# Optimization experiments

Measured on AMD Instinct MI355X. Metric: run time of the kernel, lower is better.

Reference implementation:

```python
import jax, jax.numpy as jnp
import numpy as np

B, T, E, H = 4, 2048, 4096, 128

def setup_inputs() -> dict:
    key = jax.random.key(0)
    ks = jax.random.split(key, 5)
    x = jax.random.normal(ks[0], (B, T, E), dtype=jnp.float32)
    pos_emb = jax.random.normal(ks[1], (B, T, E), dtype=jnp.float32)
    # torch nn.Linear(E, H, bias=False) weights have shape [H, E]
    scale = 1.0 / np.sqrt(E)
    Wq = jax.random.normal(ks[2], (H, E), dtype=jnp.float32) * scale
    Wk = jax.random.normal(ks[3], (H, E), dtype=jnp.float32) * scale
    Wv = jax.random.normal(ks[4], (H, E), dtype=jnp.float32) * scale
    return {"x": x, "pos_emb": pos_emb, "Wq": Wq, "Wk": Wk, "Wv": Wv}

def reference(x, pos_emb, Wq, Wk, Wv):
    Bd, Td, Ed = x.shape
    q = jnp.einsum('bte,he->bth', x, Wq)        # [B,T,H]
    k = jnp.einsum('bte,he->bth', pos_emb, Wk)  # [B,T,H] (key is computed from pos_emb, per source)
    v = jnp.einsum('bte,he->bth', x, Wv)        # [B,T,H]
    # NOTE: source scales by full model dim E**-0.5, not head_size**-0.5
    scores = jnp.einsum('bqh,bkh->bqk', q, k) * (Ed ** -0.5)  # [B,T,T]
    causal = jnp.tril(jnp.ones((Td, Td), dtype=bool))
    scores = jnp.where(causal[None, :, :], scores, -jnp.inf)
    attn = jax.nn.softmax(scores, axis=-1)
    out = jnp.einsum('bqk,bkh->bqh', attn, v)   # [B,T,H]
    return out
```

## Files before the change

### kernel.cpp

```cpp
#include <hip/hip_runtime.h>

#define BB 4
#define TT 2048
#define EE 4096
#define HH 128
#define MM (BB*TT)
#define SCALE 0.015625f

typedef short short8 __attribute__((ext_vector_type(8)));
typedef float f32x4 __attribute__((ext_vector_type(4)));

__device__ __forceinline__ unsigned short f2bf(float x) {
    unsigned int u = __float_as_uint(x);
    u = (u + 0x7fffu + ((u >> 16) & 1u)) >> 16;
    return (unsigned short)u;
}

__global__ __launch_bounds__(256) void wconv(
    const float* __restrict__ Wq, const float* __restrict__ Wk,
    const float* __restrict__ Wv, unsigned short* __restrict__ Wb)
{
    const int gid = blockIdx.x * 256 + threadIdx.x;
    const int which = gid >> 16;
    const int rem = gid & 65535;
    const float* W = (which == 0) ? Wq : (which == 1) ? Wk : Wv;
    const float4 f0 = *(const float4*)(W + (size_t)rem * 8);
    const float4 f1 = *(const float4*)(W + (size_t)rem * 8 + 4);
    short8 pk;
    pk[0] = (short)f2bf(f0.x); pk[1] = (short)f2bf(f0.y);
    pk[2] = (short)f2bf(f0.z); pk[3] = (short)f2bf(f0.w);
    pk[4] = (short)f2bf(f1.x); pk[5] = (short)f2bf(f1.y);
    pk[6] = (short)f2bf(f1.z); pk[7] = (short)f2bf(f1.w);
    *(short8*)(Wb + (size_t)which * 524288 + (size_t)rem * 8) = pk;
}

#define ASTR 72

__global__ __launch_bounds__(256) void proj_mfma(
    const float* __restrict__ x, const float* __restrict__ pe,
    const unsigned short* __restrict__ Wb,
    float* __restrict__ qo, float* __restrict__ ko_, float* __restrict__ vo)
{
    const int widx = blockIdx.y;
    const float* in = (widx == 1) ? pe : x;
    const unsigned short* W = Wb + (size_t)widx * 524288;
    float* out = (widx == 0) ? qo : (widx == 1) ? ko_ : vo;

    const int rb   = blockIdx.x * 32;
    const int tid  = threadIdx.x;
    const int lane = tid & 63, wave = tid >> 6;
    const int wr   = wave >> 1, wc = wave & 1;

    __shared__ __align__(16) unsigned short As[32 * ASTR];
    __shared__ __align__(16) unsigned short Bs[128 * ASTR];

    f32x4 acc[4];
    #pragma unroll
    for (int j = 0; j < 4; j++) acc[j] = (f32x4){0.f, 0.f, 0.f, 0.f};

    const int fr = lane & 15, ko = (lane >> 4) * 8;

    const int arow = tid >> 3, aoff = (tid & 7) * 8;
    const float* aptr = in + (size_t)(rb + arow) * EE + aoff;
    const int wrow0 = (tid)          >> 3, woff0 = ((tid) & 7) * 8;
    const int wrow1 = (tid + 256)    >> 3, woff1 = ((tid + 256) & 7) * 8;
    const int wrow2 = (tid + 512)    >> 3, woff2 = ((tid + 512) & 7) * 8;
    const int wrow3 = (tid + 768)    >> 3, woff3 = ((tid + 768) & 7) * 8;

    float4 pa0, pa1;
    short8 pw0, pw1, pw2, pw3;

    pa0 = *(const float4*)(aptr);
    pa1 = *(const float4*)(aptr + 4);
    pw0 = *(const short8*)(W + (size_t)wrow0 * EE + woff0);
    pw1 = *(const short8*)(W + (size_t)wrow1 * EE + woff1);
    pw2 = *(const short8*)(W + (size_t)wrow2 * EE + woff2);
    pw3 = *(const short8*)(W + (size_t)wrow3 * EE + woff3);

    for (int k0 = 0; k0 < EE; k0 += 64) {
        {
            short8 a;
            a[0] = (short)f2bf(pa0.x); a[1] = (short)f2bf(pa0.y);
            a[2] = (short)f2bf(pa0.z); a[3] = (short)f2bf(pa0.w);
            a[4] = (short)f2bf(pa1.x); a[5] = (short)f2bf(pa1.y);
            a[6] = (short)f2bf(pa1.z); a[7] = (short)f2bf(pa1.w);
            *(short8*)&As[arow * ASTR + aoff] = a;
            *(short8*)&Bs[wrow0 * ASTR + woff0] = pw0;
            *(short8*)&Bs[wrow1 * ASTR + woff1] = pw1;
            *(short8*)&Bs[wrow2 * ASTR + woff2] = pw2;
            *(short8*)&Bs[wrow3 * ASTR + woff3] = pw3;
        }
        __syncthreads();

        if (k0 + 64 < EE) {
            pa0 = *(const float4*)(aptr + k0 + 64);
            pa1 = *(const float4*)(aptr + k0 + 68);
            pw0 = *(const short8*)(W + (size_t)wrow0 * EE + k0 + 64 + woff0);
            pw1 = *(const short8*)(W + (size_t)wrow1 * EE + k0 + 64 + woff1);
            pw2 = *(const short8*)(W + (size_t)wrow2 * EE + k0 + 64 + woff2);
            pw3 = *(const short8*)(W + (size_t)wrow3 * EE + k0 + 64 + woff3);
        }

        #pragma unroll
        for (int kk = 0; kk < 64; kk += 32) {
            const short8 af = *(short8*)&As[(wr * 16 + fr) * ASTR + kk + ko];
            #pragma unroll
            for (int j = 0; j < 4; j++) {
                const short8 bf = *(short8*)&Bs[(wc * 64 + j * 16 + fr) * ASTR + kk + ko];
                acc[j] = __builtin_amdgcn_mfma_f32_16x16x32_bf16(af, bf, acc[j], 0, 0, 0);
            }
        }
        __syncthreads();
    }

    const int crow = (lane >> 4) * 4, ccol = lane & 15;
    #pragma unroll
    for (int j = 0; j < 4; j++)
        #pragma unroll
        for (int r = 0; r < 4; r++)
            out[(size_t)(rb + wr * 16 + crow + r) * HH + wc * 64 + j * 16 + ccol]
                = acc[j][r];
}

__global__ __launch_bounds__(256) void attn_part(
    const float* __restrict__ q, const float* __restrict__ k,
    const float* __restrict__ v,
    float* __restrict__ OP, float* __restrict__ LP)
{
    const int b    = blockIdx.z;
    const int t    = 127 - (int)blockIdx.x;
    const int s    = blockIdx.y;
    const int tid  = threadIdx.x;
    const int lane = tid & 63, wave = tid >> 6;

    const int q0 = t * 16;
    const int C  = (t + 4) >> 2;
    const int cs = (C + 1) >> 1;
    const int c0 = s ? cs : 0;
    const int c1 = s ? C  : cs;

    __shared__ float Qs[16 * 132];
    __shared__ float KVs[64 * 132];
    __shared__ float Ps[16 * 68];

    const int qb = wave * 4;
    const int kk_ = lane;
    const int hq = tid & 31, qa = tid >> 5;

    #pragma unroll
    for (int f = tid; f < 512; f += 256) {
        const int row = f >> 5, c4 = f & 31;
        *(float4*)&Qs[row * 132 + c4 * 4] =
            *(const float4*)(q + (size_t)(b * TT + q0 + row) * HH + c4 * 4);
    }

    float lacc[4] = {0.f, 0.f, 0.f, 0.f};
    float4 o0 = {0.f, 0.f, 0.f, 0.f};
    float4 o1 = {0.f, 0.f, 0.f, 0.f};

    for (int c = c0; c < c1; c++) {
        const int kb = c * 64;
        #pragma unroll
        for (int f = tid; f < 2048; f += 256) {
            const int row = f >> 5, c4 = f & 31;
            *(float4*)&KVs[row * 132 + c4 * 4] =
                *(const float4*)(k + (size_t)(b * TT + kb + row) * HH + c4 * 4);
        }
        __syncthreads();

        {
            float s0 = 0.f, s1 = 0.f, s2 = 0.f, s3 = 0.f;
            const float* Kr = &KVs[kk_ * 132];
            const float* Q0 = &Qs[(qb + 0) * 132];
            const float* Q1 = &Qs[(qb + 1) * 132];
            const float* Q2 = &Qs[(qb + 2) * 132];
            const float* Q3 = &Qs[(qb + 3) * 132];
            #pragma unroll
            for (int c4 = 0; c4 < 32; c4++) {
                const float4 kv = *(const float4*)(Kr + c4 * 4);
                float4 a;
                a = *(const float4*)(Q0 + c4 * 4);
                s0 = fmaf(a.x, kv.x, s0); s0 = fmaf(a.y, kv.y, s0);
                s0 = fmaf(a.z, kv.z, s0); s0 = fmaf(a.w, kv.w, s0);
                a = *(const float4*)(Q1 + c4 * 4);
                s1 = fmaf(a.x, kv.x, s1); s1 = fmaf(a.y, kv.y, s1);
                s1 = fmaf(a.z, kv.z, s1); s1 = fmaf(a.w, kv.w, s1);
                a = *(const float4*)(Q2 + c4 * 4);
                s2 = fmaf(a.x, kv.x, s2); s2 = fmaf(a.y, kv.y, s2);
                s2 = fmaf(a.z, kv.z, s2); s2 = fmaf(a.w, kv.w, s2);
                a = *(const float4*)(Q3 + c4 * 4);
                s3 = fmaf(a.x, kv.x, s3); s3 = fmaf(a.y, kv.y, s3);
                s3 = fmaf(a.z, kv.z, s3); s3 = fmaf(a.w, kv.w, s3);
            }
            const int gk = kb + kk_;
            float p;
            p = (gk <= q0 + qb + 0) ? __expf(s0 * SCALE) : 0.f;
            lacc[0] += p; Ps[(qb + 0) * 68 + kk_] = p;
            p = (gk <= q0 + qb + 1) ? __expf(s1 * SCALE) : 0.f;
            lacc[1] += p; Ps[(qb + 1) * 68 + kk_] = p;
            p = (gk <= q0 + qb + 2) ? __expf(s2 * SCALE) : 0.f;
            lacc[2] += p; Ps[(qb + 2) * 68 + kk_] = p;
            p = (gk <= q0 + qb + 3) ? __expf(s3 * SCALE) : 0.f;
            lacc[3] += p; Ps[(qb + 3) * 68 + kk_] = p;
        }
        __syncthreads();

        #pragma unroll
        for (int f = tid; f < 2048; f += 256) {
            const int row = f >> 5, c4 = f & 31;
            *(float4*)&KVs[row * 132 + c4 * 4] =
                *(const float4*)(v + (size_t)(b * TT + kb + row) * HH + c4 * 4);
        }
        __syncthreads();

        #pragma unroll
        for (int kk4 = 0; kk4 < 64; kk4 += 4) {
            const float4 pa = *(const float4*)&Ps[qa * 68 + kk4];
            const float4 pb = *(const float4*)&Ps[(qa + 8) * 68 + kk4];
            const float4 w0 = *(const float4*)&KVs[(kk4 + 0) * 132 + hq * 4];
            const float4 w1 = *(const float4*)&KVs[(kk4 + 1) * 132 + hq * 4];
            const float4 w2 = *(const float4*)&KVs[(kk4 + 2) * 132 + hq * 4];
            const float4 w3 = *(const float4*)&KVs[(kk4 + 3) * 132 + hq * 4];
            o0.x = fmaf(pa.x, w0.x, o0.x); o0.y = fmaf(pa.x, w0.y, o0.y);
            o0.z = fmaf(pa.x, w0.z, o0.z); o0.w = fmaf(pa.x, w0.w, o0.w);
            o0.x = fmaf(pa.y, w1.x, o0.x); o0.y = fmaf(pa.y, w1.y, o0.y);
            o0.z = fmaf(pa.y, w1.z, o0.z); o0.w = fmaf(pa.y, w1.w, o0.w);
            o0.x = fmaf(pa.z, w2.x, o0.x); o0.y = fmaf(pa.z, w2.y, o0.y);
            o0.z = fmaf(pa.z, w2.z, o0.z); o0.w = fmaf(pa.z, w2.w, o0.w);
            o0.x = fmaf(pa.w, w3.x, o0.x); o0.y = fmaf(pa.w, w3.y, o0.y);
            o0.z = fmaf(pa.w, w3.z, o0.z); o0.w = fmaf(pa.w, w3.w, o0.w);
            o1.x = fmaf(pb.x, w0.x, o1.x); o1.y = fmaf(pb.x, w0.y, o1.y);
            o1.z = fmaf(pb.x, w0.z, o1.z); o1.w = fmaf(pb.x, w0.w, o1.w);
            o1.x = fmaf(pb.y, w1.x, o1.x); o1.y = fmaf(pb.y, w1.y, o1.y);
            o1.z = fmaf(pb.y, w1.z, o1.z); o1.w = fmaf(pb.y, w1.w, o1.w);
            o1.x = fmaf(pb.z, w2.x, o1.x); o1.y = fmaf(pb.z, w2.y, o1.y);
            o1.z = fmaf(pb.z, w2.z, o1.z); o1.w = fmaf(pb.z, w2.w, o1.w);
            o1.x = fmaf(pb.w, w3.x, o1.x); o1.y = fmaf(pb.w, w3.y, o1.y);
            o1.z = fmaf(pb.w, w3.z, o1.z); o1.w = fmaf(pb.w, w3.w, o1.w);
        }
        __syncthreads();
    }

    #pragma unroll
    for (int off = 32; off > 0; off >>= 1) {
        lacc[0] += __shfl_down(lacc[0], off);
        lacc[1] += __shfl_down(lacc[1], off);
        lacc[2] += __shfl_down(lacc[2], off);
        lacc[3] += __shfl_down(lacc[3], off);
    }
    const int pbase = ((b * 128 + t) * 2 + s);
    if (lane == 0) {
        #pragma unroll
        for (int i = 0; i < 4; i++) LP[pbase * 16 + qb + i] = lacc[i];
    }
    const size_t po = (size_t)pbase * 2048;
    *(float4*)&OP[po + qa * 128 + hq * 4] = o0;
    *(float4*)&OP[po + (qa + 8) * 128 + hq * 4] = o1;
}

__global__ __launch_bounds__(256) void combine(
    const float* __restrict__ OP, const float* __restrict__ LP,
    float* __restrict__ out)
{
    const int gid = blockIdx.x * 256 + threadIdx.x;
    const int b = gid >> 16;
    const int rem = gid & 65535;
    const int qrow = rem >> 5, h4 = rem & 31;
    const int t = qrow >> 4, r = qrow & 15;
    const int base = (b * 128 + t) * 2;
    const float l = LP[(base + 0) * 16 + r] + LP[(base + 1) * 16 + r];
    const float inv = 1.f / l;
    const float4 a = ((const float4*)OP)[(size_t)(base + 0) * 512 + r * 32 + h4];
    const float4 c = ((const float4*)OP)[(size_t)(base + 1) * 512 + r * 32 + h4];
    float4 res;
    res.x = (a.x + c.x) * inv; res.y = (a.y + c.y) * inv;
    res.z = (a.z + c.z) * inv; res.w = (a.w + c.w) * inv;
    ((float4*)out)[gid] = res;
}

extern "C" void kernel_launch(void* const* d_in, const int* in_sizes, int n_in,
                              void* d_out, int out_size, void* d_ws, size_t ws_size,
                              hipStream_t stream) {
    const float* x  = (const float*)d_in[0];
    const float* pe = (const float*)d_in[1];
    const float* Wq = (const float*)d_in[2];
    const float* Wk = (const float*)d_in[3];
    const float* Wv = (const float*)d_in[4];
    float* out = (float*)d_out;

    float* qw = (float*)d_ws;
    float* kw = qw + (size_t)MM * HH;
    float* vw = kw + (size_t)MM * HH;
    unsigned short* Wb = (unsigned short*)(vw + (size_t)MM * HH);
    float* OP = (float*)(Wb + 1572864);
    float* LP = OP + 2097152;

    wconv    <<<768, 256, 0, stream>>>(Wq, Wk, Wv, Wb);
    proj_mfma<<<dim3(MM / 32, 3), 256, 0, stream>>>(x, pe, Wb, qw, kw, vw);
    attn_part<<<dim3(128, 2, BB), 256, 0, stream>>>(qw, kw, vw, OP, LP);
    combine  <<<1024, 256, 0, stream>>>(OP, LP, out);
}
```

Measured before the change: 458.9 us.

## Move attention to bf16 MFMA with transposed V and bf16 projection outputs

Replaces the scalar fp32 attention kernel with a bf16 MFMA version that uses 32-query tiles, a transposed V layout, and bf16 probability tiles. The projection kernel now writes bf16 Q/K and a transposed bf16 V, is split into two column halves for more blocks, and folds the softmax scale into Wq during weight conversion. This removes fp32 FMA-bound QK^T and PV work and halves intermediate memory traffic. The cost is extra bf16 rounding of Q/K/V and probabilities, plus less headroom against overflow because the exp is still taken without max subtraction.

```diff
diff --git a/kernel.cpp b/kernel.cpp
--- a/kernel.cpp
+++ b/kernel.cpp
@@ -9,6 +9,7 @@
 
 typedef short short8 __attribute__((ext_vector_type(8)));
 typedef float f32x4 __attribute__((ext_vector_type(4)));
+typedef unsigned short ushort_t;
 
 __device__ __forceinline__ unsigned short f2bf(float x) {
     unsigned int u = __float_as_uint(x);
@@ -18,19 +19,20 @@
 
 __global__ __launch_bounds__(256) void wconv(
     const float* __restrict__ Wq, const float* __restrict__ Wk,
-    const float* __restrict__ Wv, unsigned short* __restrict__ Wb)
+    const float* __restrict__ Wv, ushort_t* __restrict__ Wb)
 {
     const int gid = blockIdx.x * 256 + threadIdx.x;
     const int which = gid >> 16;
     const int rem = gid & 65535;
     const float* W = (which == 0) ? Wq : (which == 1) ? Wk : Wv;
+    const float sc = (which == 0) ? SCALE : 1.0f;
     const float4 f0 = *(const float4*)(W + (size_t)rem * 8);
     const float4 f1 = *(const float4*)(W + (size_t)rem * 8 + 4);
     short8 pk;
-    pk[0] = (short)f2bf(f0.x); pk[1] = (short)f2bf(f0.y);
-    pk[2] = (short)f2bf(f0.z); pk[3] = (short)f2bf(f0.w);
-    pk[4] = (short)f2bf(f1.x); pk[5] = (short)f2bf(f1.y);
-    pk[6] = (short)f2bf(f1.z); pk[7] = (short)f2bf(f1.w);
+    pk[0] = (short)f2bf(f0.x * sc); pk[1] = (short)f2bf(f0.y * sc);
+    pk[2] = (short)f2bf(f0.z * sc); pk[3] = (short)f2bf(f0.w * sc);
+    pk[4] = (short)f2bf(f1.x * sc); pk[5] = (short)f2bf(f1.y * sc);
+    pk[6] = (short)f2bf(f1.z * sc); pk[7] = (short)f2bf(f1.w * sc);
     *(short8*)(Wb + (size_t)which * 524288 + (size_t)rem * 8) = pk;
 }
 
@@ -38,44 +40,38 @@
 
 __global__ __launch_bounds__(256) void proj_mfma(
     const float* __restrict__ x, const float* __restrict__ pe,
-    const unsigned short* __restrict__ Wb,
-    float* __restrict__ qo, float* __restrict__ ko_, float* __restrict__ vo)
-{
-    const int widx = blockIdx.y;
+    const ushort_t* __restrict__ Wb,
+    ushort_t* __restrict__ qo, ushort_t* __restrict__ ko_,
+    ushort_t* __restrict__ vto)
+{
+    const int widx = blockIdx.y >> 1;
+    const int half = blockIdx.y & 1;
     const float* in = (widx == 1) ? pe : x;
-    const unsigned short* W = Wb + (size_t)widx * 524288;
-    float* out = (widx == 0) ? qo : (widx == 1) ? ko_ : vo;
+    const ushort_t* W = Wb + (size_t)widx * 524288 + (size_t)half * 64 * EE;
 
     const int rb   = blockIdx.x * 32;
     const int tid  = threadIdx.x;
     const int lane = tid & 63, wave = tid >> 6;
-    const int wr   = wave >> 1, wc = wave & 1;
-
-    __shared__ __align__(16) unsigned short As[32 * ASTR];
-    __shared__ __align__(16) unsigned short Bs[128 * ASTR];
-
-    f32x4 acc[4];
-    #pragma unroll
-    for (int j = 0; j < 4; j++) acc[j] = (f32x4){0.f, 0.f, 0.f, 0.f};
-
-    const int fr = lane & 15, ko = (lane >> 4) * 8;
+    const int wr   = wave & 1, wc = wave >> 1;
+
+    __shared__ __align__(16) ushort_t As[32 * ASTR];
+    __shared__ __align__(16) ushort_t Bs[64 * ASTR];
+
+    f32x4 acc[2];
+    acc[0] = (f32x4){0.f,0.f,0.f,0.f};
+    acc[1] = (f32x4){0.f,0.f,0.f,0.f};
+
+    const int fr = lane & 15, quad = lane >> 4, ko = quad * 8;
 
     const int arow = tid >> 3, aoff = (tid & 7) * 8;
     const float* aptr = in + (size_t)(rb + arow) * EE + aoff;
-    const int wrow0 = (tid)          >> 3, woff0 = ((tid) & 7) * 8;
-    const int wrow1 = (tid + 256)    >> 3, woff1 = ((tid + 256) & 7) * 8;
-    const int wrow2 = (tid + 512)    >> 3, woff2 = ((tid + 512) & 7) * 8;
-    const int wrow3 = (tid + 768)    >> 3, woff3 = ((tid + 768) & 7) * 8;
-
-    float4 pa0, pa1;
-    short8 pw0, pw1, pw2, pw3;
-
-    pa0 = *(const float4*)(aptr);
-    pa1 = *(const float4*)(aptr + 4);
-    pw0 = *(const short8*)(W + (size_t)wrow0 * EE + woff0);
-    pw1 = *(const short8*)(W + (size_t)wrow1 * EE + woff1);
-    pw2 = *(const short8*)(W + (size_t)wrow2 * EE + woff2);
-    pw3 = *(const short8*)(W + (size_t)wrow3 * EE + woff3);
+    const int wrow0 = tid >> 3,        woff0 = (tid & 7) * 8;
+    const int wrow1 = wrow0 + 32,      woff1 = woff0;
+
+    float4 pa0 = *(const float4*)(aptr);
+    float4 pa1 = *(const float4*)(aptr + 4);
+    short8 pw0 = *(const short8*)(W + (size_t)wrow0 * EE + woff0);
+    short8 pw1 = *(const short8*)(W + (size_t)wrow1 * EE + woff1);
 
     for (int k0 = 0; k0 < EE; k0 += 64) {
         {
@@ -87,8 +83,6 @@
             *(short8*)&As[arow * ASTR + aoff] = a;
             *(short8*)&Bs[wrow0 * ASTR + woff0] = pw0;
             *(short8*)&Bs[wrow1 * ASTR + woff1] = pw1;
-            *(short8*)&Bs[wrow2 * ASTR + woff2] = pw2;
-            *(short8*)&Bs[wrow3 * ASTR + woff3] = pw3;
         }
         __syncthreads();
 
@@ -97,165 +91,155 @@
             pa1 = *(const float4*)(aptr + k0 + 68);
             pw0 = *(const short8*)(W + (size_t)wrow0 * EE + k0 + 64 + woff0);
             pw1 = *(const short8*)(W + (size_t)wrow1 * EE + k0 + 64 + woff1);
-            pw2 = *(const short8*)(W + (size_t)wrow2 * EE + k0 + 64 + woff2);
-            pw3 = *(const short8*)(W + (size_t)wrow3 * EE + k0 + 64 + woff3);
         }
 
         #pragma unroll
         for (int kk = 0; kk < 64; kk += 32) {
             const short8 af = *(short8*)&As[(wr * 16 + fr) * ASTR + kk + ko];
             #pragma unroll
-            for (int j = 0; j < 4; j++) {
-                const short8 bf = *(short8*)&Bs[(wc * 64 + j * 16 + fr) * ASTR + kk + ko];
-                acc[j] = __builtin_amdgcn_mfma_f32_16x16x32_bf16(af, bf, acc[j], 0, 0, 0);
+            for (int t = 0; t < 2; t++) {
+                const short8 bf_ = *(short8*)&Bs[(wc * 32 + t * 16 + fr) * ASTR + kk + ko];
+                acc[t] = __builtin_amdgcn_mfma_f32_16x16x32_bf16(af, bf_, acc[t], 0, 0, 0);
             }
         }
         __syncthreads();
     }
 
-    const int crow = (lane >> 4) * 4, ccol = lane & 15;
-    #pragma unroll
-    for (int j = 0; j < 4; j++)
-        #pragma unroll
-        for (int r = 0; r < 4; r++)
-            out[(size_t)(rb + wr * 16 + crow + r) * HH + wc * 64 + j * 16 + ccol]
-                = acc[j][r];
-}
-
-__global__ __launch_bounds__(256) void attn_part(
-    const float* __restrict__ q, const float* __restrict__ k,
-    const float* __restrict__ v,
+    const int crow = quad * 4;
+    if (widx < 2) {
+        ushort_t* out = (widx == 0) ? qo : ko_;
+        #pragma unroll
+        for (int t = 0; t < 2; t++)
+            #pragma unroll
+            for (int r = 0; r < 4; r++)
+                out[(size_t)(rb + wr * 16 + crow + r) * HH
+                    + half * 64 + wc * 32 + t * 16 + fr] = f2bf(acc[t][r]);
+    } else {
+        ushort_t* T = Bs;
+        #pragma unroll
+        for (int t = 0; t < 2; t++)
+            #pragma unroll
+            for (int r = 0; r < 4; r++)
+                T[(wc * 32 + t * 16 + fr) * 40 + wr * 16 + crow + r] = f2bf(acc[t][r]);
+        __syncthreads();
+        const int h64 = tid >> 2, m0 = (tid & 3) * 8;
+        const short8 val = *(short8*)&T[h64 * 40 + m0];
+        *(short8*)(vto + (size_t)(half * 64 + h64) * MM + rb + m0) = val;
+    }
+}
+
+__global__ __launch_bounds__(256) void attn_mfma(
+    const ushort_t* __restrict__ qb, const ushort_t* __restrict__ kbf,
+    const ushort_t* __restrict__ vtb,
     float* __restrict__ OP, float* __restrict__ LP)
 {
-    const int b    = blockIdx.z;
-    const int t    = 127 - (int)blockIdx.x;
-    const int s    = blockIdx.y;
+    const int b = blockIdx.z;
+    const int s = blockIdx.y;
+    const int t = 63 - (int)blockIdx.x;
     const int tid  = threadIdx.x;
     const int lane = tid & 63, wave = tid >> 6;
-
-    const int q0 = t * 16;
-    const int C  = (t + 4) >> 2;
+    const int fr = lane & 15, quad = lane >> 4, ko = quad * 8;
+
+    const int q0 = t * 32;
+    const int C  = (t + 2) >> 1;
     const int cs = (C + 1) >> 1;
     const int c0 = s ? cs : 0;
     const int c1 = s ? C  : cs;
 
-    __shared__ float Qs[16 * 132];
-    __shared__ float KVs[64 * 132];
-    __shared__ float Ps[16 * 68];
-
-    const int qb = wave * 4;
-    const int kk_ = lane;
-    const int hq = tid & 31, qa = tid >> 5;
-
+    __shared__ __align__(16) ushort_t Qs[32 * 136];
+    __shared__ __align__(16) ushort_t Ks[64 * 136];
+    __shared__ __align__(16) ushort_t Vt[128 * 72];
+    __shared__ __align__(16) ushort_t Ps[32 * 72];
+    __shared__ float lred[2][32];
+
+    for (int f = tid; f < 512; f += 256) {
+        const int row = f >> 4, sg = f & 15;
+        *(short8*)&Qs[row * 136 + sg * 8] =
+            *(const short8*)(qb + (size_t)(b * TT + q0 + row) * HH + sg * 8);
+    }
+
+    const int rhS = (wave & 1) * 16, cqS = (wave >> 1) * 32;
+    const int rhO = (wave & 1) * 16, chO = (wave >> 1) * 64;
+
+    f32x4 oacc[4];
     #pragma unroll
-    for (int f = tid; f < 512; f += 256) {
-        const int row = f >> 5, c4 = f & 31;
-        *(float4*)&Qs[row * 132 + c4 * 4] =
-            *(const float4*)(q + (size_t)(b * TT + q0 + row) * HH + c4 * 4);
-    }
-
+    for (int i = 0; i < 4; i++) oacc[i] = (f32x4){0.f,0.f,0.f,0.f};
     float lacc[4] = {0.f, 0.f, 0.f, 0.f};
-    float4 o0 = {0.f, 0.f, 0.f, 0.f};
-    float4 o1 = {0.f, 0.f, 0.f, 0.f};
 
     for (int c = c0; c < c1; c++) {
-        const int kb = c * 64;
-        #pragma unroll
-        for (int f = tid; f < 2048; f += 256) {
-            const int row = f >> 5, c4 = f & 31;
-            *(float4*)&KVs[row * 132 + c4 * 4] =
-                *(const float4*)(k + (size_t)(b * TT + kb + row) * HH + c4 * 4);
-        }
-        __syncthreads();
-
-        {
-            float s0 = 0.f, s1 = 0.f, s2 = 0.f, s3 = 0.f;
-            const float* Kr = &KVs[kk_ * 132];
-            const float* Q0 = &Qs[(qb + 0) * 132];
-            const float* Q1 = &Qs[(qb + 1) * 132];
-            const float* Q2 = &Qs[(qb + 2) * 132];
-            const float* Q3 = &Qs[(qb + 3) * 132];
-            #pragma unroll
-            for (int c4 = 0; c4 < 32; c4++) {
-                const float4 kv = *(const float4*)(Kr + c4 * 4);
-                float4 a;
-                a = *(const float4*)(Q0 + c4 * 4);
-                s0 = fmaf(a.x, kv.x, s0); s0 = fmaf(a.y, kv.y, s0);
-                s0 = fmaf(a.z, kv.z, s0); s0 = fmaf(a.w, kv.w, s0);
-                a = *(const float4*)(Q1 + c4 * 4);
-                s1 = fmaf(a.x, kv.x, s1); s1 = fmaf(a.y, kv.y, s1);
-                s1 = fmaf(a.z, kv.z, s1); s1 = fmaf(a.w, kv.w, s1);
-                a = *(const float4*)(Q2 + c4 * 4);
-                s2 = fmaf(a.x, kv.x, s2); s2 = fmaf(a.y, kv.y, s2);
-                s2 = fmaf(a.z, kv.z, s2); s2 = fmaf(a.w, kv.w, s2);
-                a = *(const float4*)(Q3 + c4 * 4);
-                s3 = fmaf(a.x, kv.x, s3); s3 = fmaf(a.y, kv.y, s3);
-                s3 = fmaf(a.z, kv.z, s3); s3 = fmaf(a.w, kv.w, s3);
+        const int kb_ = c * 64;
+        for (int f = tid; f < 1024; f += 256) {
+            const int row = f >> 4, sg = f & 15;
+            *(short8*)&Ks[row * 136 + sg * 8] =
+                *(const short8*)(kbf + (size_t)(b * TT + kb_ + row) * HH + sg * 8);
+        }
+        for (int f = tid; f < 1024; f += 256) {
+            const int h = f >> 3, sg = f & 7;
+            *(short8*)&Vt[h * 72 + sg * 8] =
+                *(const short8*)(vtb + (size_t)h * MM + b * TT + kb_ + sg * 8);
+        }
+        __syncthreads();
+
+        f32x4 sacc[2];
+        sacc[0] = (f32x4){0.f,0.f,0.f,0.f};
+        sacc[1] = (f32x4){0.f,0.f,0.f,0.f};
+        #pragma unroll
+        for (int kk = 0; kk < 128; kk += 32) {
+            const short8 af = *(short8*)&Qs[(rhS + fr) * 136 + kk + ko];
+            const short8 b0 = *(short8*)&Ks[(cqS + fr) * 136 + kk + ko];
+            const short8 b1 = *(short8*)&Ks[(cqS + 16 + fr) * 136 + kk + ko];
+            sacc[0] = __builtin_amdgcn_mfma_f32_16x16x32_bf16(af, b0, sacc[0], 0, 0, 0);
+            sacc[1] = __builtin_amdgcn_mfma_f32_16x16x32_bf16(af, b1, sacc[1], 0, 0, 0);
+        }
+
+        #pragma unroll
+        for (int tl = 0; tl < 2; tl++)
+            #pragma unroll
+            for (int r = 0; r < 4; r++) {
+                const int row = rhS + quad * 4 + r;
+                const int col = cqS + tl * 16 + fr;
+                const float p = ((kb_ + col) <= (q0 + row)) ? __expf(sacc[tl][r]) : 0.f;
+                lacc[r] += p;
+                Ps[row * 72 + col] = f2bf(p);
             }
-            const int gk = kb + kk_;
-            float p;
-            p = (gk <= q0 + qb + 0) ? __expf(s0 * SCALE) : 0.f;
-            lacc[0] += p; Ps[(qb + 0) * 68 + kk_] = p;
-            p = (gk <= q0 + qb + 1) ? __expf(s1 * SCALE) : 0.f;
-            lacc[1] += p; Ps[(qb + 1) * 68 + kk_] = p;
-            p = (gk <= q0 + qb + 2) ? __expf(s2 * SCALE) : 0.f;
-            lacc[2] += p; Ps[(qb + 2) * 68 + kk_] = p;
-            p = (gk <= q0 + qb + 3) ? __expf(s3 * SCALE) : 0.f;
-            lacc[3] += p; Ps[(qb + 3) * 68 + kk_] = p;
-        }
-        __syncthreads();
-
-        #pragma unroll
-        for (int f = tid; f < 2048; f += 256) {
-            const int row = f >> 5, c4 = f & 31;
-            *(float4*)&KVs[row * 132 + c4 * 4] =
-                *(const float4*)(v + (size_t)(b * TT + kb + row) * HH + c4 * 4);
-        }
-        __syncthreads();
-
-        #pragma unroll
-        for (int kk4 = 0; kk4 < 64; kk4 += 4) {
-            const float4 pa = *(const float4*)&Ps[qa * 68 + kk4];
-            const float4 pb = *(const float4*)&Ps[(qa + 8) * 68 + kk4];
-            const float4 w0 = *(const float4*)&KVs[(kk4 + 0) * 132 + hq * 4];
-            const float4 w1 = *(const float4*)&KVs[(kk4 + 1) * 132 + hq * 4];
-            const float4 w2 = *(const float4*)&KVs[(kk4 + 2) * 132 + hq * 4];
-            const float4 w3 = *(const float4*)&KVs[(kk4 + 3) * 132 + hq * 4];
-            o0.x = fmaf(pa.x, w0.x, o0.x); o0.y = fmaf(pa.x, w0.y, o0.y);
-            o0.z = fmaf(pa.x, w0.z, o0.z); o0.w = fmaf(pa.x, w0.w, o0.w);
-            o0.x = fmaf(pa.y, w1.x, o0.x); o0.y = fmaf(pa.y, w1.y, o0.y);
-            o0.z = fmaf(pa.y, w1.z, o0.z); o0.w = fmaf(pa.y, w1.w, o0.w);
-            o0.x = fmaf(pa.z, w2.x, o0.x); o0.y = fmaf(pa.z, w2.y, o0.y);
-            o0.z = fmaf(pa.z, w2.z, o0.z); o0.w = fmaf(pa.z, w2.w, o0.w);
-            o0.x = fmaf(pa.w, w3.x, o0.x); o0.y = fmaf(pa.w, w3.y, o0.y);
-            o0.z = fmaf(pa.w, w3.z, o0.z); o0.w = fmaf(pa.w, w3.w, o0.w);
-            o1.x = fmaf(pb.x, w0.x, o1.x); o1.y = fmaf(pb.x, w0.y, o1.y);
-            o1.z = fmaf(pb.x, w0.z, o1.z); o1.w = fmaf(pb.x, w0.w, o1.w);
-            o1.x = fmaf(pb.y, w1.x, o1.x); o1.y = fmaf(pb.y, w1.y, o1.y);
-            o1.z = fmaf(pb.y, w1.z, o1.z); o1.w = fmaf(pb.y, w1.w, o1.w);
-            o1.x = fmaf(pb.z, w2.x, o1.x); o1.y = fmaf(pb.z, w2.y, o1.y);
-            o1.z = fmaf(pb.z, w2.z, o1.z); o1.w = fmaf(pb.z, w2.w, o1.w);
-            o1.x = fmaf(pb.w, w3.x, o1.x); o1.y = fmaf(pb.w, w3.y, o1.y);
-            o1.z = fmaf(pb.w, w3.z, o1.z); o1.w = fmaf(pb.w, w3.w, o1.w);
+        __syncthreads();
+
+        #pragma unroll
+        for (int ks = 0; ks < 64; ks += 32) {
+            const short8 af = *(short8*)&Ps[(rhO + fr) * 72 + ks + ko];
+            #pragma unroll
+            for (int tl = 0; tl < 4; tl++) {
+                const short8 bf_ = *(short8*)&Vt[(chO + tl * 16 + fr) * 72 + ks + ko];
+                oacc[tl] = __builtin_amdgcn_mfma_f32_16x16x32_bf16(af, bf_, oacc[tl], 0, 0, 0);
+            }
         }
         __syncthreads();
     }
 
     #pragma unroll
-    for (int off = 32; off > 0; off >>= 1) {
-        lacc[0] += __shfl_down(lacc[0], off);
-        lacc[1] += __shfl_down(lacc[1], off);
-        lacc[2] += __shfl_down(lacc[2], off);
-        lacc[3] += __shfl_down(lacc[3], off);
-    }
-    const int pbase = ((b * 128 + t) * 2 + s);
-    if (lane == 0) {
-        #pragma unroll
-        for (int i = 0; i < 4; i++) LP[pbase * 16 + qb + i] = lacc[i];
-    }
-    const size_t po = (size_t)pbase * 2048;
-    *(float4*)&OP[po + qa * 128 + hq * 4] = o0;
-    *(float4*)&OP[po + (qa + 8) * 128 + hq * 4] = o1;
+    for (int r = 0; r < 4; r++) {
+        float v = lacc[r];
+        #pragma unroll
+        for (int m = 1; m < 16; m <<= 1) v += __shfl_xor(v, m);
+        lacc[r] = v;
+    }
+    if (fr == 0) {
+        #pragma unroll
+        for (int r = 0; r < 4; r++)
+            lred[wave >> 1][rhS + quad * 4 + r] = lacc[r];
+    }
+    __syncthreads();
+    const int pbase = ((b * 64 + t) * 2 + s);
+    if (tid < 32) LP[(size_t)pbase * 32 + tid] = lred[0][tid] + lred[1][tid];
+
+    #pragma unroll
+    for (int tl = 0; tl < 4; tl++)
+        #pragma unroll
+        for (int r = 0; r < 4; r++) {
+            const int row = rhO + quad * 4 + r;
+            const int col = chO + tl * 16 + fr;
+            OP[(size_t)pbase * 4096 + row * 128 + col] = oacc[tl][r];
+        }
 }
 
 __global__ __launch_bounds__(256) void combine(
@@ -266,12 +250,12 @@
     const int b = gid >> 16;
     const int rem = gid & 65535;
     const int qrow = rem >> 5, h4 = rem & 31;
-    const int t = qrow >> 4, r = qrow & 15;
-    const int base = (b * 128 + t) * 2;
-    const float l = LP[(base + 0) * 16 + r] + LP[(base + 1) * 16 + r];
+    const int t = qrow >> 5, r = qrow & 31;
+    const int base = (b * 64 + t) * 2;
+    const float l = LP[(size_t)base * 32 + r] + LP[(size_t)(base + 1) * 32 + r];
     const float inv = 1.f / l;
-    const float4 a = ((const float4*)OP)[(size_t)(base + 0) * 512 + r * 32 + h4];
-    const float4 c = ((const float4*)OP)[(size_t)(base + 1) * 512 + r * 32 + h4];
+    const float4 a = ((const float4*)OP)[(size_t)base * 1024 + r * 32 + h4];
+    const float4 c = ((const float4*)OP)[(size_t)(base + 1) * 1024 + r * 32 + h4];
     float4 res;
     res.x = (a.x + c.x) * inv; res.y = (a.y + c.y) * inv;
     res.z = (a.z + c.z) * inv; res.w = (a.w + c.w) * inv;
@@ -288,15 +272,15 @@
     const float* Wv = (const float*)d_in[4];
     float* out = (float*)d_out;
 
-    float* qw = (float*)d_ws;
-    float* kw = qw + (size_t)MM * HH;
-    float* vw = kw + (size_t)MM * HH;
-    unsigned short* Wb = (unsigned short*)(vw + (size_t)MM * HH);
-    float* OP = (float*)(Wb + 1572864);
-    float* LP = OP + 2097152;
+    ushort_t* qb  = (ushort_t*)d_ws;
+    ushort_t* kbf = qb  + (size_t)MM * HH;
+    ushort_t* vtb = kbf + (size_t)MM * HH;
+    ushort_t* Wb  = vtb + (size_t)MM * HH;
+    float* OP = (float*)(Wb + (size_t)3 * 128 * 4096);
+    float* LP = OP + (size_t)512 * 4096;
 
     wconv    <<<768, 256, 0, stream>>>(Wq, Wk, Wv, Wb);
-    proj_mfma<<<dim3(MM / 32, 3), 256, 0, stream>>>(x, pe, Wb, qw, kw, vw);
-    attn_part<<<dim3(128, 2, BB), 256, 0, stream>>>(qw, kw, vw, OP, LP);
+    proj_mfma<<<dim3(256, 6), 256, 0, stream>>>(x, pe, Wb, qb, kbf, vtb);
+    attn_mfma<<<dim3(64, 2, BB), 256, 0, stream>>>(qb, kbf, vtb, OP, LP);
     combine  <<<1024, 256, 0, stream>>>(OP, LP, out);
 }
```

After: 393.0 us. 1.17x faster.
